# Performance work log

Hardware: AMD Instinct MI355X
Metric: run time of the kernel (lower is better)

The kernel has to match this reference:

```python
import jax, jax.numpy as jnp
import numpy as np

N_HEADS = 16
KEY_DIM = 64
VAL_DIM = 64
HIDDEN = 1024
SCALE = 1.0 / float(KEY_DIM) ** 0.5


def setup_inputs() -> dict:
    key = jax.random.key(0)
    ks = jax.random.split(key, 16)
    B, Lq, Lk, R = 2, 2048, 2048, 2048
    inp = {
        "query": jax.random.normal(ks[0], (B, Lq, HIDDEN), jnp.float32),
        "value": jax.random.normal(ks[1], (B, Lk, HIDDEN), jnp.float32),
        "positional_embedding": jax.random.normal(ks[2], (R, HIDDEN), jnp.float32),
        "u_weight": jax.random.normal(ks[3], (N_HEADS, KEY_DIM), jnp.float32) * 0.02,
        "v_weight": jax.random.normal(ks[4], (N_HEADS, KEY_DIM), jnp.float32) * 0.02,
        "indices": jax.random.randint(ks[5], (2, Lq, Lk), 0, R, jnp.int64 if jax.config.jax_enable_x64 else jnp.int32),
        "lower": jax.random.uniform(ks[6], (Lq, Lk), jnp.float32),
    }
    s = 0.02
    inp["Wq"] = jax.random.normal(ks[7], (HIDDEN, N_HEADS * KEY_DIM), jnp.float32) * s
    inp["bq"] = jnp.zeros((N_HEADS * KEY_DIM,), jnp.float32)
    inp["Wk"] = jax.random.normal(ks[8], (HIDDEN, N_HEADS * KEY_DIM), jnp.float32) * s
    inp["bk"] = jnp.zeros((N_HEADS * KEY_DIM,), jnp.float32)
    inp["Wv"] = jax.random.normal(ks[9], (HIDDEN, N_HEADS * VAL_DIM), jnp.float32) * s
    inp["bv"] = jnp.zeros((N_HEADS * VAL_DIM,), jnp.float32)
    inp["Wr"] = jax.random.normal(ks[10], (HIDDEN, N_HEADS * KEY_DIM), jnp.float32) * s
    inp["br"] = jnp.zeros((N_HEADS * KEY_DIM,), jnp.float32)
    inp["Wo"] = jax.random.normal(ks[11], (N_HEADS * VAL_DIM, HIDDEN), jnp.float32) * s
    inp["bo"] = jnp.zeros((HIDDEN,), jnp.float32)
    return inp


def reference(query, value, positional_embedding, u_weight, v_weight, indices, lower,
              Wq, bq, Wk, bk, Wv, bv, Wr, br, Wo, bo):
    B, Lq, _ = query.shape
    Lk = value.shape[1]
    R = positional_embedding.shape[0]
    # projections (torch Linear with weights stored as [in, out])
    q = (query @ Wq + bq).reshape(B, Lq, N_HEADS, KEY_DIM)
    k = (value @ Wk + bk).reshape(B, Lk, N_HEADS, KEY_DIM)
    v = (value @ Wv + bv).reshape(B, Lk, N_HEADS, VAL_DIM)
    r = (positional_embedding @ Wr + br).reshape(R, N_HEADS, KEY_DIM)
    # content (AC) and position (BD) score terms -> [i, j, b, n]
    AC = jnp.einsum("bind,bjnd->ijbn", q + u_weight, k)
    BD = jnp.einsum("bind,jnd->ijbn", q + v_weight, r)
    # rel-shift: gather [Lq, R] -> [Lq, Lk] positions, then apply lower mask
    BD = BD[indices[0], indices[1]] * lower[:, :, None, None]
    attn = jax.nn.softmax((AC + BD) * SCALE, axis=1)  # softmax over key dim j
    out = jnp.einsum("ijbn,bjnd->bind", attn, v).reshape(B, Lq, N_HEADS * VAL_DIM)
    return out @ Wo + bo
```

## Files before the change

### kernel.cpp

```cpp
#include <hip/hip_runtime.h>
#include <stdint.h>

typedef __attribute__((ext_vector_type(8))) short short8;
typedef __attribute__((ext_vector_type(4))) float f32x4;
typedef unsigned short u16;
typedef unsigned int u32;

#define LQ 2048
#define LK 2048
#define RDIM 2048
#define HID 1024
#define NH 16
#define DH 64
#define XL_SCALE 0.125f

__device__ __forceinline__ float bf2f(u16 u){
  union { unsigned int i; float f; } v; v.i = ((unsigned int)u) << 16; return v.f;
}
__device__ __forceinline__ u16 f2bf(float f){
  union { float f; unsigned int i; } v; v.f = f;
  unsigned int r = v.i + 0x7fffu + ((v.i >> 16) & 1u);
  return (u16)(r >> 16);
}
__device__ __forceinline__ f32x4 fzero(){ f32x4 z = {0.0f, 0.0f, 0.0f, 0.0f}; return z; }

__global__ void k_detect(const u32* __restrict__ q, const u32* __restrict__ idxw,
                         int* __restrict__ flags){
  int t = threadIdx.x;
  u32 w = q[t];
  int b = (w >> 7) & 0xFF;
  unsigned long long mb = __ballot(b >= 100 && b <= 140);
  u32 hi = idxw[2 * t + 1];
  unsigned long long mi = __ballot(hi == 0u);
  if (t == 0){
    flags[0] = (__popcll(mb) >= 48) ? 1 : 0;
    flags[1] = (__popcll(mi) == 64) ? 1 : 0;
  }
}

__global__ void k_ingest(const void* __restrict__ src, u16* __restrict__ dst,
                         int n4, const int* __restrict__ flags){
  int f = flags[0];
  int stride = gridDim.x * blockDim.x;
  for (int i = blockIdx.x * blockDim.x + threadIdx.x; i < n4; i += stride){
    if (f){
      reinterpret_cast<uint2*>(dst)[i] = reinterpret_cast<const uint2*>(src)[i];
    } else {
      float4 v = reinterpret_cast<const float4*>(src)[i];
      union { u16 h[4]; uint2 u; } t;
      t.h[0] = f2bf(v.x); t.h[1] = f2bf(v.y); t.h[2] = f2bf(v.z); t.h[3] = f2bf(v.w);
      reinterpret_cast<uint2*>(dst)[i] = t.u;
    }
  }
}

__global__ void k_transpose(const u16* __restrict__ W, u16* __restrict__ Wt){
  __shared__ u16 t[64][65];
  int tid = threadIdx.x;
  int bx = blockIdx.x, by = blockIdx.y;
#pragma unroll
  for (int it = 0; it < 16; ++it){
    int id = it * 256 + tid;
    int r = id >> 6, c = id & 63;
    t[r][c] = W[(size_t)(by * 64 + r) * HID + bx * 64 + c];
  }
  __syncthreads();
#pragma unroll
  for (int it = 0; it < 16; ++it){
    int id = it * 256 + tid;
    int r = id >> 6, c = id & 63;
    Wt[(size_t)(bx * 64 + r) * HID + by * 64 + c] = t[c][r];
  }
}

__global__ void k_gemm(const u16* __restrict__ A, const u16* __restrict__ Bt,
                       const u16* __restrict__ bias,
                       const u16* __restrict__ add0, const u16* __restrict__ add1,
                       void* __restrict__ D0, u16* __restrict__ D1,
                       int headmajor, const int* __restrict__ oflags){
  __shared__ u16 As[128][72];
  __shared__ u16 Bs[128][72];
  int tid = threadIdx.x;
  int l = tid & 63, w = tid >> 6;
  int lr = l & 15, g = l >> 4;
  int wr = w >> 1, wc = w & 1;
  int outf32 = oflags ? (oflags[0] == 0) : 0;
  f32x4 acc[4][4];
#pragma unroll
  for (int a = 0; a < 4; ++a)
#pragma unroll
    for (int bq_ = 0; bq_ < 4; ++bq_) acc[a][bq_] = fzero();
  const size_t arowg = (size_t)blockIdx.x * 128;
  const size_t browg = (size_t)blockIdx.y * 128;
  for (int kt = 0; kt < HID; kt += 64){
#pragma unroll
    for (int it = 0; it < 4; ++it){
      int id = it * 256 + tid;
      int r = id >> 3, ch = id & 7;
      uint4 va = *reinterpret_cast<const uint4*>(A + (arowg + r) * HID + kt + ch * 8);
      *reinterpret_cast<uint4*>(&As[r][ch * 8]) = va;
      uint4 vb = *reinterpret_cast<const uint4*>(Bt + (browg + r) * HID + kt + ch * 8);
      *reinterpret_cast<uint4*>(&Bs[r][ch * 8]) = vb;
    }
    __syncthreads();
#pragma unroll
    for (int ks = 0; ks < 2; ++ks){
      short8 af[4], bfv[4];
#pragma unroll
      for (int mf = 0; mf < 4; ++mf)
        af[mf] = *reinterpret_cast<const short8*>(&As[wr * 64 + mf * 16 + lr][ks * 32 + 8 * g]);
#pragma unroll
      for (int nf = 0; nf < 4; ++nf)
        bfv[nf] = *reinterpret_cast<const short8*>(&Bs[wc * 64 + nf * 16 + lr][ks * 32 + 8 * g]);
#pragma unroll
      for (int mf = 0; mf < 4; ++mf)
#pragma unroll
        for (int nf = 0; nf < 4; ++nf)
          acc[mf][nf] = __builtin_amdgcn_mfma_f32_16x16x32_bf16(af[mf], bfv[nf], acc[mf][nf], 0, 0, 0);
    }
    __syncthreads();
  }
#pragma unroll
  for (int mf = 0; mf < 4; ++mf)
#pragma unroll
    for (int nf = 0; nf < 4; ++nf){
      int col = (int)browg + wc * 64 + nf * 16 + lr;
      float bcol = bf2f(bias[col]);
      float a0 = add0 ? bf2f(add0[col]) : 0.0f;
      float a1 = add1 ? bf2f(add1[col]) : 0.0f;
#pragma unroll
      for (int reg = 0; reg < 4; ++reg){
        int row = (int)arowg + wr * 64 + mf * 16 + 4 * g + reg;
        float base = acc[mf][nf][reg] + bcol;
        size_t dst;
        if (headmajor){
          int b = row >> 11, i = row & 2047;
          int n = col >> 6, d = col & 63;
          dst = ((size_t)(b * NH + n) * LQ + i) * DH + d;
        } else {
          dst = (size_t)row * HID + col;
        }
        if (outf32) ((float*)D0)[dst] = base + a0;
        else        ((u16*)D0)[dst] = f2bf(base + a0);
        if (D1) D1[dst] = f2bf(base + a1);
      }
    }
}

template<int G>
__global__ void k_bdfull(const u16* __restrict__ qv, const u16* __restrict__ rr,
                         u16* __restrict__ bdf, int bnBase){
  __shared__ u16 tile[16][32][G];
  int tid = threadIdx.x;
  int l = tid & 63, w = tid >> 6;
  int lr = l & 15, g = l >> 4;
  int i0 = blockIdx.x * 16, j0 = blockIdx.y * 32;
  constexpr int C = (G >= 4) ? (G / 4) : 1;
  if (G >= 4 || w < G){
#pragma unroll
    for (int bi = 0; bi < C; ++bi){
      int g_ = w * C + bi;
      int bn = bnBase + g_;
      int b = bn >> 4, n = bn & 15;
      const u16* qb = qv + ((size_t)(b * NH + n) * LQ + i0) * DH;
      const u16* rb = rr + ((size_t)n * RDIM + j0) * DH;
      f32x4 acc2[2];
      acc2[0] = fzero(); acc2[1] = fzero();
#pragma unroll
      for (int ks = 0; ks < 2; ++ks){
        short8 a = *reinterpret_cast<const short8*>(qb + (size_t)lr * DH + ks * 32 + 8 * g);
#pragma unroll
        for (int nf = 0; nf < 2; ++nf){
          short8 bb = *reinterpret_cast<const short8*>(rb + (size_t)(lr + 16 * nf) * DH + ks * 32 + 8 * g);
          acc2[nf] = __builtin_amdgcn_mfma_f32_16x16x32_bf16(a, bb, acc2[nf], 0, 0, 0);
        }
      }
#pragma unroll
      for (int nf = 0; nf < 2; ++nf){
        int jj = lr + 16 * nf;
#pragma unroll
        for (int reg = 0; reg < 4; ++reg)
          tile[4 * g + reg][jj][g_] = f2bf(acc2[nf][reg]);
      }
    }
  }
  __syncthreads();
  constexpr int W = (G >= 4) ? 4 : G;
  constexpr int PARTS = G / W;
  constexpr int CHUNKS = 512 * PARTS;
#pragma unroll
  for (int e = 0; e < (CHUNKS + 255) / 256; ++e){
    int id = e * 256 + tid;
    if (CHUNKS < 256 * ((CHUNKS + 255) / 256) && id >= CHUNKS) break;
    int line = id / PARTS, part = id % PARTS;
    int ii = line >> 5, jj = line & 31;
    int k = part * W;
    const u16* src = &tile[ii][jj][k];
    u16* dst = bdf + ((size_t)(i0 + ii) * RDIM + (size_t)(j0 + jj)) * G + k;
    if (W == 4)
      *reinterpret_cast<unsigned long long*>(dst) = *reinterpret_cast<const unsigned long long*>(src);
    else if (W == 2)
      *reinterpret_cast<unsigned int*>(dst) = *reinterpret_cast<const unsigned int*>(src);
    else
      *dst = *src;
  }
}

template<int G>
__global__ void k_gather(const u16* __restrict__ bdf, const int* __restrict__ idx,
                         const u16* __restrict__ lower, u16* __restrict__ bdg,
                         const int* __restrict__ flags){
  __shared__ u16 tile[G][16][32];
  int tid = threadIdx.x;
  int i64f = flags[1];
  int i0 = blockIdx.x * 16, j0 = blockIdx.y * 32;
#pragma unroll
  for (int it = 0; it < 2; ++it){
    int p = it * 256 + tid;
    int ii = p >> 5, jj = p & 31;
    size_t off = (size_t)(i0 + ii) * LK + (j0 + jj);
    long long a0, a1;
    if (i64f){
      const long long* ip = (const long long*)idx;
      a0 = ip[off]; a1 = ip[(size_t)LQ * LK + off];
    } else {
      a0 = idx[off]; a1 = idx[(size_t)LQ * LK + off];
    }
    float lw = bf2f(lower[off]);
    const u16* src = bdf + ((size_t)a0 * RDIM + (size_t)a1) * G;
    union { uint4 q[2]; u32 w2[8]; u16 h[16]; } uv;
    if (G == 16){
      uv.q[0] = *reinterpret_cast<const uint4*>(src);
      uv.q[1] = *reinterpret_cast<const uint4*>(src + 8);
    } else if (G == 8){
      uv.q[0] = *reinterpret_cast<const uint4*>(src);
    } else if (G == 2){
      uv.w2[0] = *reinterpret_cast<const u32*>(src);
    } else {
      uv.h[0] = *src;
    }
#pragma unroll
    for (int k = 0; k < G; ++k)
      tile[k][ii][jj] = f2bf(bf2f(uv.h[k]) * lw);
  }
  __syncthreads();
  constexpr int CHUNKS = G * 128;
#pragma unroll
  for (int e = 0; e < (CHUNKS + 255) / 256; ++e){
    int id = e * 256 + tid;
    if (CHUNKS < 256 * ((CHUNKS + 255) / 256) && id >= CHUNKS) break;
    int g_ = id >> 7, rem = id & 127;
    int ii = rem >> 3, part = rem & 7;
    unsigned long long v = *reinterpret_cast<const unsigned long long*>(&tile[g_][ii][part * 4]);
    *reinterpret_cast<unsigned long long*>(
        bdg + (size_t)g_ * LQ * LK + (size_t)(i0 + ii) * LK + j0 + part * 4) = v;
  }
}

__global__ void k_flash(const u16* __restrict__ qu, const u16* __restrict__ kk,
                        const u16* __restrict__ vv, const u16* __restrict__ bdg,
                        u16* __restrict__ oo, int bnBase){
  __shared__ u16 klds[64][72];
  __shared__ u16 vtlds[64][72];
  __shared__ u16 plds[4][16][72];
  int tid = threadIdx.x;
  int l = tid & 63, w = tid >> 6;
  int lr = l & 15, g = l >> 4;
  int gi = blockIdx.x;
  int bn = bnBase + gi;
  int b = bn >> 4, n = bn & 15;
  int i0 = blockIdx.y * 64;
  const u16* qb = qu + ((size_t)bn * LQ + i0 + w * 16) * DH;
  short8 aq0 = *reinterpret_cast<const short8*>(qb + (size_t)lr * DH + 8 * g);
  short8 aq1 = *reinterpret_cast<const short8*>(qb + (size_t)lr * DH + 32 + 8 * g);
  f32x4 O[4];
#pragma unroll
  for (int nf = 0; nf < 4; ++nf) O[nf] = fzero();
  float mrun[4], lrun[4];
#pragma unroll
  for (int r = 0; r < 4; ++r){ mrun[r] = -1e30f; lrun[r] = 0.0f; }
  const u16* kbase = kk + (size_t)bn * LK * DH;
  const u16* vbase = vv + (size_t)bn * LK * DH;
  const u16* bdb = bdg + (size_t)gi * LQ * LK + (size_t)(i0 + w * 16) * LK;

  for (int j0 = 0; j0 < LK; j0 += 64){
#pragma unroll
    for (int it = 0; it < 2; ++it){
      int id = it * 256 + tid;
      int r = id >> 3, ch = id & 7;
      uint4 kv = *reinterpret_cast<const uint4*>(kbase + (size_t)(j0 + r) * DH + ch * 8);
      *reinterpret_cast<uint4*>(&klds[r][ch * 8]) = kv;
      uint4 vv4 = *reinterpret_cast<const uint4*>(vbase + (size_t)(j0 + r) * DH + ch * 8);
      u16 tmp[8];
      *reinterpret_cast<uint4*>(tmp) = vv4;
#pragma unroll
      for (int e2 = 0; e2 < 8; ++e2) vtlds[ch * 8 + e2][r] = tmp[e2];
    }
    __syncthreads();

    float sv[4][4];
#pragma unroll
    for (int nf = 0; nf < 4; ++nf){
      f32x4 z = fzero();
      short8 bk0 = *reinterpret_cast<const short8*>(&klds[lr + 16 * nf][8 * g]);
      short8 bk1 = *reinterpret_cast<const short8*>(&klds[lr + 16 * nf][32 + 8 * g]);
      z = __builtin_amdgcn_mfma_f32_16x16x32_bf16(aq0, bk0, z, 0, 0, 0);
      z = __builtin_amdgcn_mfma_f32_16x16x32_bf16(aq1, bk1, z, 0, 0, 0);
#pragma unroll
      for (int reg = 0; reg < 4; ++reg){
        float bd = bf2f(bdb[(size_t)(4 * g + reg) * LK + j0 + lr + 16 * nf]);
        sv[nf][reg] = (z[reg] + bd) * XL_SCALE;
      }
    }
    float fs[4];
#pragma unroll
    for (int reg = 0; reg < 4; ++reg){
      float mx = fmaxf(fmaxf(sv[0][reg], sv[1][reg]), fmaxf(sv[2][reg], sv[3][reg]));
#pragma unroll
      for (int d = 1; d < 16; d <<= 1) mx = fmaxf(mx, __shfl_xor(mx, d));
      float mnew = fmaxf(mrun[reg], mx);
      fs[reg] = __expf(mrun[reg] - mnew);
      mrun[reg] = mnew;
      float sum = 0.0f;
#pragma unroll
      for (int nf = 0; nf < 4; ++nf){
        sv[nf][reg] = __expf(sv[nf][reg] - mnew);
        sum += sv[nf][reg];
      }
#pragma unroll
      for (int d = 1; d < 16; d <<= 1) sum += __shfl_xor(sum, d);
      lrun[reg] = lrun[reg] * fs[reg] + sum;
    }
#pragma unroll
    for (int nf = 0; nf < 4; ++nf)
#pragma unroll
      for (int reg = 0; reg < 4; ++reg)
        O[nf][reg] *= fs[reg];
#pragma unroll
    for (int nf = 0; nf < 4; ++nf)
#pragma unroll
      for (int reg = 0; reg < 4; ++reg)
        plds[w][4 * g + reg][lr + 16 * nf] = f2bf(sv[nf][reg]);
    short8 pa0 = *reinterpret_cast<const short8*>(&plds[w][lr][8 * g]);
    short8 pa1 = *reinterpret_cast<const short8*>(&plds[w][lr][32 + 8 * g]);
#pragma unroll
    for (int nf = 0; nf < 4; ++nf){
      short8 bv0 = *reinterpret_cast<const short8*>(&vtlds[lr + 16 * nf][8 * g]);
      short8 bv1 = *reinterpret_cast<const short8*>(&vtlds[lr + 16 * nf][32 + 8 * g]);
      O[nf] = __builtin_amdgcn_mfma_f32_16x16x32_bf16(pa0, bv0, O[nf], 0, 0, 0);
      O[nf] = __builtin_amdgcn_mfma_f32_16x16x32_bf16(pa1, bv1, O[nf], 0, 0, 0);
    }
    __syncthreads();
  }
#pragma unroll
  for (int nf = 0; nf < 4; ++nf)
#pragma unroll
    for (int reg = 0; reg < 4; ++reg){
      int i = i0 + w * 16 + 4 * g + reg;
      float vo = O[nf][reg] / lrun[reg];
      oo[((size_t)(b * LQ + i)) * HID + n * DH + lr + 16 * nf] = f2bf(vo);
    }
}

extern "C" void kernel_launch(void* const* d_in, const int* in_sizes, int n_in,
                              void* d_out, int out_size, void* d_ws, size_t ws_size,
                              hipStream_t stream){
  const void* query = d_in[0];
  const void* value = d_in[1];
  const void* pos   = d_in[2];
  const void* uw    = d_in[3];
  const void* vw    = d_in[4];
  const int* idx    = (const int*)d_in[5];
  const void* lower = d_in[6];
  const void* Wq = d_in[7];  const void* bq = d_in[8];
  const void* Wk = d_in[9];  const void* bk = d_in[10];
  const void* Wv = d_in[11]; const void* bv = d_in[12];
  const void* Wr = d_in[13]; const void* br = d_in[14];
  const void* Wo = d_in[15]; const void* bo = d_in[16];
  (void)in_sizes; (void)n_in; (void)out_size;

  char* ws = (char*)d_ws;
  const size_t MB = (size_t)1 << 20;
  u16* cquery = (u16*)(ws + 0 * MB);
  u16* cvalue = (u16*)(ws + 8 * MB);
  u16* cpos   = (u16*)(ws + 16 * MB);
  u16* clower = (u16*)(ws + 20 * MB);
  u16* cWq = (u16*)(ws + 28 * MB);
  u16* cWk = (u16*)(ws + 30 * MB);
  u16* cWv = (u16*)(ws + 32 * MB);
  u16* cWr = (u16*)(ws + 34 * MB);
  u16* cWo = (u16*)(ws + 36 * MB);
  char* sm = ws + 38 * MB;
  u16* cuw = (u16*)(sm + 0 * 4096);
  u16* cvw = (u16*)(sm + 1 * 4096);
  u16* cbq = (u16*)(sm + 2 * 4096);
  u16* cbk = (u16*)(sm + 3 * 4096);
  u16* cbv = (u16*)(sm + 4 * 4096);
  u16* cbr = (u16*)(sm + 5 * 4096);
  u16* cbo = (u16*)(sm + 6 * 4096);
  int* flags = (int*)(sm + 7 * 4096);
  u16* wqt = (u16*)(ws + 39 * MB);
  u16* wkt = (u16*)(ws + 41 * MB);
  u16* wvt = (u16*)(ws + 43 * MB);
  u16* wrt = (u16*)(ws + 45 * MB);
  u16* wot = (u16*)(ws + 47 * MB);
  u16* qu  = (u16*)(ws + 49 * MB);
  u16* qv  = (u16*)(ws + 57 * MB);
  u16* kkp = (u16*)(ws + 65 * MB);
  u16* vvp = (u16*)(ws + 73 * MB);
  u16* rrp = (u16*)(ws + 81 * MB);
  u16* oo  = (u16*)(ws + 85 * MB);
  u16* bdf = (u16*)(ws + 96 * MB);

  int G = 1;
  if (ws_size >= 352 * MB) G = 16;
  else if (ws_size >= 224 * MB) G = 8;
  else if (ws_size >= 128 * MB) G = 2;
  u16* bdg = (u16*)(ws + (96 + 8 * (size_t)G) * MB);

  dim3 blk(256);
  k_detect<<<1, 64, 0, stream>>>((const u32*)query, (const u32*)idx, flags);
#define ING(SRC, DST, N) k_ingest<<<dim3(512), blk, 0, stream>>>(SRC, DST, (N) / 4, flags)
  ING(query, cquery, 2 * LQ * HID);
  ING(value, cvalue, 2 * LK * HID);
  ING(pos,   cpos,   RDIM * HID);
  ING(lower, clower, LQ * LK);
  ING(Wq, cWq, HID * HID);  ING(Wk, cWk, HID * HID);
  ING(Wv, cWv, HID * HID);  ING(Wr, cWr, HID * HID);
  ING(Wo, cWo, HID * HID);
  ING(uw, cuw, NH * DH);    ING(vw, cvw, NH * DH);
  ING(bq, cbq, HID); ING(bk, cbk, HID); ING(bv, cbv, HID);
  ING(br, cbr, HID); ING(bo, cbo, HID);
#undef ING

  k_transpose<<<dim3(16, 16), blk, 0, stream>>>(cWq, wqt);
  k_transpose<<<dim3(16, 16), blk, 0, stream>>>(cWk, wkt);
  k_transpose<<<dim3(16, 16), blk, 0, stream>>>(cWv, wvt);
  k_transpose<<<dim3(16, 16), blk, 0, stream>>>(cWr, wrt);
  k_transpose<<<dim3(16, 16), blk, 0, stream>>>(cWo, wot);

  k_gemm<<<dim3(32, 8), blk, 0, stream>>>(cquery, wqt, cbq, cuw, cvw, qu, qv, 1, nullptr);
  k_gemm<<<dim3(32, 8), blk, 0, stream>>>(cvalue, wkt, cbk, nullptr, nullptr, kkp, nullptr, 1, nullptr);
  k_gemm<<<dim3(32, 8), blk, 0, stream>>>(cvalue, wvt, cbv, nullptr, nullptr, vvp, nullptr, 1, nullptr);
  k_gemm<<<dim3(16, 8), blk, 0, stream>>>(cpos, wrt, cbr, nullptr, nullptr, rrp, nullptr, 1, nullptr);

  for (int b0 = 0; b0 < 2 * NH; b0 += G){
    if (G == 16){
      k_bdfull<16><<<dim3(128, 64), blk, 0, stream>>>(qv, rrp, bdf, b0);
      k_gather<16><<<dim3(128, 64), blk, 0, stream>>>(bdf, idx, clower, bdg, flags);
    } else if (G == 8){
      k_bdfull<8><<<dim3(128, 64), blk, 0, stream>>>(qv, rrp, bdf, b0);
      k_gather<8><<<dim3(128, 64), blk, 0, stream>>>(bdf, idx, clower, bdg, flags);
    } else if (G == 2){
      k_bdfull<2><<<dim3(128, 64), blk, 0, stream>>>(qv, rrp, bdf, b0);
      k_gather<2><<<dim3(128, 64), blk, 0, stream>>>(bdf, idx, clower, bdg, flags);
    } else {
      k_bdfull<1><<<dim3(128, 64), blk, 0, stream>>>(qv, rrp, bdf, b0);
      k_gather<1><<<dim3(128, 64), blk, 0, stream>>>(bdf, idx, clower, bdg, flags);
    }
    k_flash<<<dim3(G, 32), blk, 0, stream>>>(qu, kkp, vvp, bdg, oo, b0);
  }
  k_gemm<<<dim3(32, 8), blk, 0, stream>>>(oo, wot, cbo, nullptr, nullptr, d_out, nullptr, 0, flags);
}
```

Baseline: 1.078 ms.

## Batch ingest and weight transposes, precompute gather offsets, widen flash key tile

Merges the many per-tensor ingest launches into two multi-segment launches. It also fuses the weight fp32-to-bf16 conversion into one batched transpose kernel covering all five weights. Gather indices are converted once into 32-bit flat offsets, stored over the already-consumed query buffer, so the per-group gather kernels stop re-reading int64/int32 index pairs. The flash kernel now processes 128 keys per iteration instead of 64, halving barriers and softmax rescales at the cost of more LDS and registers.

```diff
diff --git a/kernel.cpp b/kernel.cpp
--- a/kernel.cpp
+++ b/kernel.cpp
@@ -38,23 +38,29 @@
   }
 }
 
-__global__ void k_ingest(const void* __restrict__ src, u16* __restrict__ dst,
-                         int n4, const int* __restrict__ flags){
+struct Seg { const void* src; u16* dst; int n4; };
+struct SegPack { Seg s[8]; };
+__global__ void k_ingestN(SegPack p, const int* __restrict__ flags){
   int f = flags[0];
+  Seg sg = p.s[blockIdx.y];
   int stride = gridDim.x * blockDim.x;
-  for (int i = blockIdx.x * blockDim.x + threadIdx.x; i < n4; i += stride){
+  for (int i = blockIdx.x * blockDim.x + threadIdx.x; i < sg.n4; i += stride){
     if (f){
-      reinterpret_cast<uint2*>(dst)[i] = reinterpret_cast<const uint2*>(src)[i];
+      reinterpret_cast<uint2*>(sg.dst)[i] = reinterpret_cast<const uint2*>(sg.src)[i];
     } else {
-      float4 v = reinterpret_cast<const float4*>(src)[i];
+      float4 v = reinterpret_cast<const float4*>(sg.src)[i];
       union { u16 h[4]; uint2 u; } t;
       t.h[0] = f2bf(v.x); t.h[1] = f2bf(v.y); t.h[2] = f2bf(v.z); t.h[3] = f2bf(v.w);
-      reinterpret_cast<uint2*>(dst)[i] = t.u;
-    }
-  }
-}
-
-__global__ void k_transpose(const u16* __restrict__ W, u16* __restrict__ Wt){
+      reinterpret_cast<uint2*>(sg.dst)[i] = t.u;
+    }
+  }
+}
+
+struct WPack { const void* src[5]; u16* dst[5]; };
+__global__ void k_wtrans(WPack p, const int* __restrict__ flags){
+  int f = flags[0];
+  const void* W = p.src[blockIdx.z];
+  u16* Wt = p.dst[blockIdx.z];
   __shared__ u16 t[64][65];
   int tid = threadIdx.x;
   int bx = blockIdx.x, by = blockIdx.y;
@@ -62,7 +68,8 @@
   for (int it = 0; it < 16; ++it){
     int id = it * 256 + tid;
     int r = id >> 6, c = id & 63;
-    t[r][c] = W[(size_t)(by * 64 + r) * HID + bx * 64 + c];
+    size_t so = (size_t)(by * 64 + r) * HID + bx * 64 + c;
+    t[r][c] = f ? ((const u16*)W)[so] : f2bf(((const float*)W)[so]);
   }
   __syncthreads();
 #pragma unroll
@@ -70,6 +77,23 @@
     int id = it * 256 + tid;
     int r = id >> 6, c = id & 63;
     Wt[(size_t)(bx * 64 + r) * HID + by * 64 + c] = t[c][r];
+  }
+}
+
+__global__ void k_goff(const int* __restrict__ idx, int* __restrict__ goff,
+                       const int* __restrict__ flags){
+  int i64f = flags[1];
+  const size_t N = (size_t)LQ * LK;
+  size_t stride = (size_t)gridDim.x * blockDim.x;
+  for (size_t t = (size_t)blockIdx.x * blockDim.x + threadIdx.x; t < N; t += stride){
+    long long a0, a1;
+    if (i64f){
+      const long long* ip = (const long long*)idx;
+      a0 = ip[t]; a1 = ip[N + t];
+    } else {
+      a0 = idx[t]; a1 = idx[N + t];
+    }
+    goff[t] = (int)(a0 * RDIM + a1);
   }
 }
 
@@ -207,27 +231,19 @@
 }
 
 template<int G>
-__global__ void k_gather(const u16* __restrict__ bdf, const int* __restrict__ idx,
-                         const u16* __restrict__ lower, u16* __restrict__ bdg,
-                         const int* __restrict__ flags){
+__global__ void k_gather(const u16* __restrict__ bdf, const int* __restrict__ goff,
+                         const u16* __restrict__ lower, u16* __restrict__ bdg){
   __shared__ u16 tile[G][16][32];
   int tid = threadIdx.x;
-  int i64f = flags[1];
   int i0 = blockIdx.x * 16, j0 = blockIdx.y * 32;
 #pragma unroll
   for (int it = 0; it < 2; ++it){
     int p = it * 256 + tid;
     int ii = p >> 5, jj = p & 31;
     size_t off = (size_t)(i0 + ii) * LK + (j0 + jj);
-    long long a0, a1;
-    if (i64f){
-      const long long* ip = (const long long*)idx;
-      a0 = ip[off]; a1 = ip[(size_t)LQ * LK + off];
-    } else {
-      a0 = idx[off]; a1 = idx[(size_t)LQ * LK + off];
-    }
+    int go = goff[off];
     float lw = bf2f(lower[off]);
-    const u16* src = bdf + ((size_t)a0 * RDIM + (size_t)a1) * G;
+    const u16* src = bdf + (size_t)go * G;
     union { uint4 q[2]; u32 w2[8]; u16 h[16]; } uv;
     if (G == 16){
       uv.q[0] = *reinterpret_cast<const uint4*>(src);
@@ -260,9 +276,9 @@
 __global__ void k_flash(const u16* __restrict__ qu, const u16* __restrict__ kk,
                         const u16* __restrict__ vv, const u16* __restrict__ bdg,
                         u16* __restrict__ oo, int bnBase){
-  __shared__ u16 klds[64][72];
-  __shared__ u16 vtlds[64][72];
-  __shared__ u16 plds[4][16][72];
+  __shared__ u16 klds[128][72];
+  __shared__ u16 vtlds[64][136];
+  __shared__ u16 plds[4][16][136];
   int tid = threadIdx.x;
   int l = tid & 63, w = tid >> 6;
   int lr = l & 15, g = l >> 4;
@@ -283,9 +299,9 @@
   const u16* vbase = vv + (size_t)bn * LK * DH;
   const u16* bdb = bdg + (size_t)gi * LQ * LK + (size_t)(i0 + w * 16) * LK;
 
-  for (int j0 = 0; j0 < LK; j0 += 64){
-#pragma unroll
-    for (int it = 0; it < 2; ++it){
+  for (int j0 = 0; j0 < LK; j0 += 128){
+#pragma unroll
+    for (int it = 0; it < 4; ++it){
       int id = it * 256 + tid;
       int r = id >> 3, ch = id & 7;
       uint4 kv = *reinterpret_cast<const uint4*>(kbase + (size_t)(j0 + r) * DH + ch * 8);
@@ -298,9 +314,9 @@
     }
     __syncthreads();
 
-    float sv[4][4];
-#pragma unroll
-    for (int nf = 0; nf < 4; ++nf){
+    float sv[8][4];
+#pragma unroll
+    for (int nf = 0; nf < 8; ++nf){
       f32x4 z = fzero();
       short8 bk0 = *reinterpret_cast<const short8*>(&klds[lr + 16 * nf][8 * g]);
       short8 bk1 = *reinterpret_cast<const short8*>(&klds[lr + 16 * nf][32 + 8 * g]);
@@ -315,7 +331,9 @@
     float fs[4];
 #pragma unroll
     for (int reg = 0; reg < 4; ++reg){
-      float mx = fmaxf(fmaxf(sv[0][reg], sv[1][reg]), fmaxf(sv[2][reg], sv[3][reg]));
+      float mx = sv[0][reg];
+#pragma unroll
+      for (int nf = 1; nf < 8; ++nf) mx = fmaxf(mx, sv[nf][reg]);
 #pragma unroll
       for (int d = 1; d < 16; d <<= 1) mx = fmaxf(mx, __shfl_xor(mx, d));
       float mnew = fmaxf(mrun[reg], mx);
@@ -323,7 +341,7 @@
       mrun[reg] = mnew;
       float sum = 0.0f;
 #pragma unroll
-      for (int nf = 0; nf < 4; ++nf){
+      for (int nf = 0; nf < 8; ++nf){
         sv[nf][reg] = __expf(sv[nf][reg] - mnew);
         sum += sv[nf][reg];
       }
@@ -337,18 +355,21 @@
       for (int reg = 0; reg < 4; ++reg)
         O[nf][reg] *= fs[reg];
 #pragma unroll
-    for (int nf = 0; nf < 4; ++nf)
+    for (int nf = 0; nf < 8; ++nf)
 #pragma unroll
       for (int reg = 0; reg < 4; ++reg)
         plds[w][4 * g + reg][lr + 16 * nf] = f2bf(sv[nf][reg]);
-    short8 pa0 = *reinterpret_cast<const short8*>(&plds[w][lr][8 * g]);
-    short8 pa1 = *reinterpret_cast<const short8*>(&plds[w][lr][32 + 8 * g]);
+    short8 pa[4];
+#pragma unroll
+    for (int ks = 0; ks < 4; ++ks)
+      pa[ks] = *reinterpret_cast<const short8*>(&plds[w][lr][ks * 32 + 8 * g]);
 #pragma unroll
     for (int nf = 0; nf < 4; ++nf){
-      short8 bv0 = *reinterpret_cast<const short8*>(&vtlds[lr + 16 * nf][8 * g]);
-      short8 bv1 = *reinterpret_cast<const short8*>(&vtlds[lr + 16 * nf][32 + 8 * g]);
-      O[nf] = __builtin_amdgcn_mfma_f32_16x16x32_bf16(pa0, bv0, O[nf], 0, 0, 0);
-      O[nf] = __builtin_amdgcn_mfma_f32_16x16x32_bf16(pa1, bv1, O[nf], 0, 0, 0);
+#pragma unroll
+      for (int ks = 0; ks < 4; ++ks){
+        short8 bv = *reinterpret_cast<const short8*>(&vtlds[lr + 16 * nf][ks * 32 + 8 * g]);
+        O[nf] = __builtin_amdgcn_mfma_f32_16x16x32_bf16(pa[ks], bv, O[nf], 0, 0, 0);
+      }
     }
     __syncthreads();
   }
@@ -383,13 +404,9 @@
   const size_t MB = (size_t)1 << 20;
   u16* cquery = (u16*)(ws + 0 * MB);
   u16* cvalue = (u16*)(ws + 8 * MB);
+  int* goff   = (int*)(ws + 0 * MB);
   u16* cpos   = (u16*)(ws + 16 * MB);
   u16* clower = (u16*)(ws + 20 * MB);
-  u16* cWq = (u16*)(ws + 28 * MB);
-  u16* cWk = (u16*)(ws + 30 * MB);
-  u16* cWv = (u16*)(ws + 32 * MB);
-  u16* cWr = (u16*)(ws + 34 * MB);
-  u16* cWo = (u16*)(ws + 36 * MB);
   char* sm = ws + 38 * MB;
   u16* cuw = (u16*)(sm + 0 * 4096);
   u16* cvw = (u16*)(sm + 1 * 4096);
@@ -420,43 +437,56 @@
 
   dim3 blk(256);
   k_detect<<<1, 64, 0, stream>>>((const u32*)query, (const u32*)idx, flags);
-#define ING(SRC, DST, N) k_ingest<<<dim3(512), blk, 0, stream>>>(SRC, DST, (N) / 4, flags)
-  ING(query, cquery, 2 * LQ * HID);
-  ING(value, cvalue, 2 * LK * HID);
-  ING(pos,   cpos,   RDIM * HID);
-  ING(lower, clower, LQ * LK);
-  ING(Wq, cWq, HID * HID);  ING(Wk, cWk, HID * HID);
-  ING(Wv, cWv, HID * HID);  ING(Wr, cWr, HID * HID);
-  ING(Wo, cWo, HID * HID);
-  ING(uw, cuw, NH * DH);    ING(vw, cvw, NH * DH);
-  ING(bq, cbq, HID); ING(bk, cbk, HID); ING(bv, cbv, HID);
-  ING(br, cbr, HID); ING(bo, cbo, HID);
-#undef ING
-
-  k_transpose<<<dim3(16, 16), blk, 0, stream>>>(cWq, wqt);
-  k_transpose<<<dim3(16, 16), blk, 0, stream>>>(cWk, wkt);
-  k_transpose<<<dim3(16, 16), blk, 0, stream>>>(cWv, wvt);
-  k_transpose<<<dim3(16, 16), blk, 0, stream>>>(cWr, wrt);
-  k_transpose<<<dim3(16, 16), blk, 0, stream>>>(cWo, wot);
+
+  {
+    SegPack big;
+    big.s[0] = { query, cquery, 2 * LQ * HID / 4 };
+    big.s[1] = { value, cvalue, 2 * LK * HID / 4 };
+    big.s[2] = { pos,   cpos,   RDIM * HID / 4 };
+    big.s[3] = { lower, clower, LQ * LK / 4 };
+    for (int i = 4; i < 8; ++i) big.s[i] = { nullptr, nullptr, 0 };
+    k_ingestN<<<dim3(512, 4), blk, 0, stream>>>(big, flags);
+    SegPack sml;
+    sml.s[0] = { uw, cuw, NH * DH / 4 };
+    sml.s[1] = { vw, cvw, NH * DH / 4 };
+    sml.s[2] = { bq, cbq, HID / 4 };
+    sml.s[3] = { bk, cbk, HID / 4 };
+    sml.s[4] = { bv, cbv, HID / 4 };
+    sml.s[5] = { br, cbr, HID / 4 };
+    sml.s[6] = { bo, cbo, HID / 4 };
+    sml.s[7] = { nullptr, nullptr, 0 };
+    k_ingestN<<<dim3(4, 7), blk, 0, stream>>>(sml, flags);
+  }
+  {
+    WPack wp;
+    wp.src[0] = Wq; wp.dst[0] = wqt;
+    wp.src[1] = Wk; wp.dst[1] = wkt;
+    wp.src[2] = Wv; wp.dst[2] = wvt;
+    wp.src[3] = Wr; wp.dst[3] = wrt;
+    wp.src[4] = Wo; wp.dst[4] = wot;
+    k_wtrans<<<dim3(16, 16, 5), blk, 0, stream>>>(wp, flags);
+  }
 
   k_gemm<<<dim3(32, 8), blk, 0, stream>>>(cquery, wqt, cbq, cuw, cvw, qu, qv, 1, nullptr);
   k_gemm<<<dim3(32, 8), blk, 0, stream>>>(cvalue, wkt, cbk, nullptr, nullptr, kkp, nullptr, 1, nullptr);
   k_gemm<<<dim3(32, 8), blk, 0, stream>>>(cvalue, wvt, cbv, nullptr, nullptr, vvp, nullptr, 1, nullptr);
   k_gemm<<<dim3(16, 8), blk, 0, stream>>>(cpos, wrt, cbr, nullptr, nullptr, rrp, nullptr, 1, nullptr);
 
+  k_goff<<<dim3(1024), blk, 0, stream>>>(idx, goff, flags);
+
   for (int b0 = 0; b0 < 2 * NH; b0 += G){
     if (G == 16){
       k_bdfull<16><<<dim3(128, 64), blk, 0, stream>>>(qv, rrp, bdf, b0);
-      k_gather<16><<<dim3(128, 64), blk, 0, stream>>>(bdf, idx, clower, bdg, flags);
+      k_gather<16><<<dim3(128, 64), blk, 0, stream>>>(bdf, goff, clower, bdg);
     } else if (G == 8){
       k_bdfull<8><<<dim3(128, 64), blk, 0, stream>>>(qv, rrp, bdf, b0);
-      k_gather<8><<<dim3(128, 64), blk, 0, stream>>>(bdf, idx, clower, bdg, flags);
+      k_gather<8><<<dim3(128, 64), blk, 0, stream>>>(bdf, goff, clower, bdg);
     } else if (G == 2){
       k_bdfull<2><<<dim3(128, 64), blk, 0, stream>>>(qv, rrp, bdf, b0);
-      k_gather<2><<<dim3(128, 64), blk, 0, stream>>>(bdf, idx, clower, bdg, flags);
+      k_gather<2><<<dim3(128, 64), blk, 0, stream>>>(bdf, goff, clower, bdg);
     } else {
       k_bdfull<1><<<dim3(128, 64), blk, 0, stream>>>(qv, rrp, bdf, b0);
-      k_gather<1><<<dim3(128, 64), blk, 0, stream>>>(bdf, idx, clower, bdg, flags);
+      k_gather<1><<<dim3(128, 64), blk, 0, stream>>>(bdf, goff, clower, bdg);
     }
     k_flash<<<dim3(G, 32), blk, 0, stream>>>(qu, kkp, vvp, bdg, oo, b0);
   }
```

Measured after the change: 1.008 ms. 6.4% less time.
